# Optimization experiments

Hardware: AMD Instinct MI355X
Metric: run time of the kernel (lower is better)

The kernel has to match this reference:

```python
import jax, jax.numpy as jnp
import numpy as np

L, N, D, B_, T = 4, 4, 2048, 2, 2048  # num_blocks, expansion_rate, dim, batch, seq


def setup_inputs() -> dict:
    key = jax.random.key(0)
    ks = jax.random.split(key, 12)
    f = lambda k, sh, s=0.02: s * jax.random.normal(k, sh, jnp.float32)
    x = jax.random.normal(ks[0], (B_, T, D), jnp.float32)
    # structural torch inits + small noise so grads/kernels are exercised
    eyecols = jnp.stack([jnp.eye(N, dtype=jnp.float32)[:, [i % N]] for i in range(L)])  # [L,N,1]
    A_m = eyecols + f(ks[1], (L, N, 1), 0.05)
    A_r = jnp.broadcast_to(jnp.eye(N, dtype=jnp.float32), (L, N, N)) + f(ks[2], (L, N, N), 0.05)
    Bp = jnp.ones((L, 1, N), jnp.float32) + f(ks[3], (L, 1, N), 0.05)
    W_m = f(ks[4], (L, D, 1))
    W_r = f(ks[5], (L, D, N))
    W_b = f(ks[6], (L, D, N))
    s_a = 0.01 * jnp.ones((L, 1, 1), jnp.float32)
    s_b = 0.01 * jnp.ones((L, 1, 1), jnp.float32)
    dyn_gamma = jnp.ones((L, D), jnp.float32) + f(ks[7], (L, D), 0.05)   # LayerNorm(bias=False)
    norm_gamma = jnp.ones((L, D), jnp.float32) + f(ks[8], (L, D), 0.05)  # per-block norm weight
    norm_beta = f(ks[9], (L, D))                                          # per-block norm bias
    Wblk = f(ks[10], (L, D, D), 1.0) / np.sqrt(D)                         # block = Linear(D, D)
    bblk = f(ks[11], (L, D))
    return dict(x=x, A_m=A_m, A_r=A_r, Bp=Bp, W_m=W_m, W_r=W_r, W_b=W_b,
                s_a=s_a, s_b=s_b, dyn_gamma=dyn_gamma, norm_gamma=norm_gamma,
                norm_beta=norm_beta, Wblk=Wblk, bblk=bblk)


def _ln(x, gamma, beta=None, eps=1e-5):
    mu = jnp.mean(x, axis=-1, keepdims=True)
    var = jnp.mean(jnp.square(x - mu), axis=-1, keepdims=True)
    y = (x - mu) * jax.lax.rsqrt(var + eps) * gamma
    return y if beta is None else y + beta


def reference(x, A_m, A_r, Bp, W_m, W_r, W_b, s_a, s_b,
              dyn_gamma, norm_gamma, norm_beta, Wblk, bblk):
    # hyper branch (n > 0), dynamic=True, pre_norm=True
    H = jnp.repeat(x[:, :, None, :], N, axis=2)  # [B,T,N,D]
    for i in range(L):
        # ---- width connections ----
        Hn = _ln(H, dyn_gamma[i])                                              # dynamic LN, no bias
        Am = A_m[i] + s_a[i] * jnp.tanh(jnp.einsum('btnd,do->btno', Hn, W_m[i]))  # [B,T,N,1]
        Ar = A_r[i] + s_a[i] * jnp.tanh(jnp.einsum('btnd,dm->btnm', Hn, W_r[i]))  # [B,T,N,N]
        WC = jnp.concatenate([Am, Ar], axis=-1)                                # [B,T,N,1+N]
        Ht = jnp.einsum('btnd,btnm->btdm', H, WC)                              # H^T @ WC
        h = Ht[..., 0]                                                         # [B,T,D]
        H = jnp.swapaxes(Ht[..., 1:], -2, -1)                                  # [B,T,N,D]
        # ---- pre-norm + block ----
        h = _ln(h, norm_gamma[i], norm_beta[i])
        h = jnp.einsum('btd,de->bte', h, Wblk[i]) + bblk[i]
        # ---- depth connections ----
        hn = _ln(h, dyn_gamma[i])
        Bv = Bp[i][0] + s_b[i] * jnp.tanh(jnp.einsum('btd,dn->btn', hn, W_b[i]))  # [B,T,N]
        H = H + h[:, :, None, :] * Bv[..., None]
    return H.sum(axis=2)  # [B,T,D]
```

## Files before the change

kernel.cpp:

```cpp
#include <hip/hip_runtime.h>
#include <hip/hip_bf16.h>


#define DD 2048
#define NN 4
#define LL 4
#define NTOK 4096
#define EPSF 1e-5f
#define STS 80

typedef __attribute__((ext_vector_type(8))) short bf16x8;
typedef __attribute__((ext_vector_type(4))) float f32x4;
typedef __attribute__((ext_vector_type(2))) float f32x2;

__device__ __forceinline__ float bf2f(short u) {
  union { unsigned int i; float f; } v;
  v.i = ((unsigned int)(unsigned short)u) << 16;
  return v.f;
}
__device__ __forceinline__ short f2bf(float f) {
  __hip_bfloat16 h = __float2bfloat16(f);
  short s;
  __builtin_memcpy(&s, &h, 2);
  return s;
}
__device__ __forceinline__ float wred(float v) {
#pragma unroll
  for (int off = 32; off > 0; off >>= 1) v += __shfl_xor(v, off, 64);
  return v;
}
__device__ __forceinline__ void ld16(const void* g, void* l) {
  __builtin_amdgcn_global_load_lds(
      (const __attribute__((address_space(1))) void*)g,
      (__attribute__((address_space(3))) void*)l, 16, 0, 0);
}
__host__ __device__ constexpr int pofs(int k, int l) {
  return k == 0 ? 20 + l * 5
       : k == 1 ? 40 + (l - 1) * 5
       : k == 2 ? 55 + (l - 2) * 5
                : 65;
}

__global__ __launch_bounds__(256) void prep_pack(
    const float* __restrict__ W_m, const float* __restrict__ W_r,
    const float* __restrict__ W_b, const float* __restrict__ dyn_gamma,
    const float* __restrict__ norm_gamma, const float* __restrict__ norm_beta,
    short* __restrict__ gwm, short* __restrict__ gwr, short* __restrict__ gwb,
    float* __restrict__ rb) {
  const int i = blockIdx.x * 256 + threadIdx.x;
  const float g = dyn_gamma[i];
  gwm[i] = f2bf(g * W_m[i]);
  f32x4 r = *(const f32x4*)(W_r + (size_t)i * 4);
  f32x4 b = *(const f32x4*)(W_b + (size_t)i * 4);
  short ro[4], bo[4];
#pragma unroll
  for (int k = 0; k < 4; k++) { ro[k] = f2bf(g * r[k]); bo[k] = f2bf(g * b[k]); }
  *(unsigned long long*)(gwr + (size_t)i * 4) = *(unsigned long long*)ro;
  *(unsigned long long*)(gwb + (size_t)i * 4) = *(unsigned long long*)bo;
  rb[i] = norm_beta[i] / norm_gamma[i];
}

__global__ __launch_bounds__(64) void prep_sums(
    const float* __restrict__ W_m, const float* __restrict__ W_r,
    const float* __restrict__ W_b, const float* __restrict__ dyn_gamma,
    float* __restrict__ S0w, float* __restrict__ T0d) {
  const int l = blockIdx.x;
  const int lane = threadIdx.x;
  float s[5] = {0, 0, 0, 0, 0}, t[4] = {0, 0, 0, 0};
  for (int d = lane; d < DD; d += 64) {
    const float g = dyn_gamma[l * DD + d];
    s[0] += g * W_m[l * DD + d];
    f32x4 r = *(const f32x4*)(W_r + ((size_t)l * DD + d) * 4);
    f32x4 b = *(const f32x4*)(W_b + ((size_t)l * DD + d) * 4);
#pragma unroll
    for (int m = 0; m < 4; m++) { s[1 + m] += g * r[m]; t[m] += g * b[m]; }
  }
#pragma unroll
  for (int m = 0; m < 5; m++) s[m] = wred(s[m]);
#pragma unroll
  for (int n = 0; n < 4; n++) t[n] = wred(t[n]);
  if (lane == 0) {
#pragma unroll
    for (int m = 0; m < 5; m++) S0w[l * 5 + m] = s[m];
#pragma unroll
    for (int n = 0; n < 4; n++) T0d[l * 4 + n] = t[n];
  }
}

__global__ __launch_bounds__(256) void transpose_wblk(
    const float* __restrict__ W, const float* __restrict__ norm_gamma,
    short* __restrict__ Wt) {
  __shared__ float tile[64][65];
  const int blk = blockIdx.z;
  const int c0 = blockIdx.x * 64;
  const int r0 = blockIdx.y * 64;
  const float* Ws = W + (size_t)blk * DD * DD;
  short* Wd = Wt + (size_t)blk * DD * DD;
  const int tx = threadIdx.x & 63, ty = threadIdx.x >> 6;
#pragma unroll
  for (int r = 0; r < 16; r++) {
    const int row = ty + r * 4;
    tile[row][tx] = Ws[(size_t)(r0 + row) * DD + c0 + tx];
  }
  const float gsc = norm_gamma[blk * DD + r0 + tx];
  __syncthreads();
#pragma unroll
  for (int r = 0; r < 16; r++) {
    const int row = ty + r * 4;
    Wd[(size_t)(c0 + row) * DD + r0 + tx] = f2bf(tile[tx][row] * gsc);
  }
}

__global__ __launch_bounds__(256) void row_sums(
    const short* __restrict__ Wt, const float* __restrict__ rb,
    const float* __restrict__ bblk, float* __restrict__ E0,
    float* __restrict__ E1) {
  const int l = blockIdx.y;
  const int e = blockIdx.x * 4 + (threadIdx.x >> 6);
  const int lane = threadIdx.x & 63;
  const short* row = Wt + ((size_t)l * DD + e) * DD;
  const float* rbl = rb + l * DD;
  float s1 = 0.f, s0 = 0.f;
#pragma unroll
  for (int it = 0; it < 4; it++) {
    const int d0 = lane * 8 + it * 512;
    bf16x8 w = *(const bf16x8*)(row + d0);
    f32x4 r0 = *(const f32x4*)(rbl + d0), r1 = *(const f32x4*)(rbl + d0 + 4);
#pragma unroll
    for (int q = 0; q < 8; q++) {
      const float wq = bf2f(w[q]);
      s1 += wq;
      s0 += wq * ((q < 4) ? r0[q] : r1[q - 4]);
    }
  }
  s1 = wred(s1); s0 = wred(s0);
  if (lane == 0) {
    E1[l * DD + e] = s1;
    E0[l * DD + e] = s0 + bblk[l * DD + e];
  }
}

__global__ __launch_bounds__(256) void width0_kernel(
    const float* __restrict__ x, short* __restrict__ b0,
    short* __restrict__ hout, f32x2* __restrict__ tst, float* __restrict__ Cc,
    float* __restrict__ ST, const float* __restrict__ A_m,
    const float* __restrict__ A_r, const short* __restrict__ gwm,
    const short* __restrict__ gwr, const float* __restrict__ s_a,
    const float* __restrict__ S0w) {
  const int wave = threadIdx.x >> 6;
  const int lane = threadIdx.x & 63;
  const int tok = blockIdx.x * 4 + wave;
  const float* xr = x + (size_t)tok * DD;
  short* b0t = b0 + (size_t)tok * DD;

  bf16x8 xb[4];
#pragma unroll
  for (int j = 0; j < 4; j++) {
    const int d0 = lane * 8 + j * 512;
    f32x4 a = *(const f32x4*)(xr + d0);
    f32x4 b = *(const f32x4*)(xr + d0 + 4);
    bf16x8 p;
#pragma unroll
    for (int q = 0; q < 4; q++) { p[q] = f2bf(a[q]); p[4 + q] = f2bf(b[q]); }
    xb[j] = p;
    *(bf16x8*)(b0t + d0) = p;
  }

  float o = 0.f, qq = 0.f, P0[4][5];
#pragma unroll
  for (int l = 0; l < 4; l++)
#pragma unroll
    for (int m = 0; m < 5; m++) P0[l][m] = 0.f;

#pragma unroll
  for (int j = 0; j < 4; j++) {
    const int d0 = lane * 8 + j * 512;
    bf16x8 wmv[4], wrv[4][4];
#pragma unroll
    for (int l = 0; l < 4; l++) {
      wmv[l] = *(const bf16x8*)(gwm + l * DD + d0);
#pragma unroll
      for (int p = 0; p < 4; p++)
        wrv[l][p] = *(const bf16x8*)(gwr + ((size_t)l * DD + d0 + 2 * p) * 4);
    }
#pragma unroll
    for (int q = 0; q < 8; q++) {
      const float hv = bf2f(xb[j][q]);
      o += hv; qq += hv * hv;
#pragma unroll
      for (int l = 0; l < 4; l++) {
        P0[l][0] += hv * bf2f(wmv[l][q]);
#pragma unroll
        for (int m = 0; m < 4; m++)
          P0[l][1 + m] += hv * bf2f(wrv[l][q >> 1][(q & 1) * 4 + m]);
      }
    }
  }
  o = wred(o); qq = wred(qq);
#pragma unroll
  for (int l = 0; l < 4; l++)
#pragma unroll
    for (int m = 0; m < 5; m++) P0[l][m] = wred(P0[l][m]);

  const float sa = s_a[0];
  const float mu = o * (1.f / DD);
  const float inv = rsqrtf(qq * (1.f / DD) - mu * mu + EPSF);
  const float t0 = tanhf(inv * (P0[0][0] - mu * S0w[0]));
  float tm[4];
#pragma unroll
  for (int m = 0; m < 4; m++)
    tm[m] = tanhf(inv * (P0[0][1 + m] - mu * S0w[1 + m]));
  float amSum = 0.f, arCol[4] = {0, 0, 0, 0};
#pragma unroll
  for (int n = 0; n < 4; n++) {
    amSum += A_m[n] + sa * t0;
#pragma unroll
    for (int m = 0; m < 4; m++) arCol[m] += A_r[n * 4 + m] + sa * tm[m];
  }

  if (lane == 0) {
    const float sh = amSum * o;
    const float sh2 = amSum * amSum * qq;
    const float mu2 = sh * (1.f / DD);
    const float inv2 = rsqrtf(sh2 * (1.f / DD) - mu2 * mu2 + EPSF);
    f32x2 t; t[0] = inv2; t[1] = mu2 * inv2;
    tst[tok] = t;
    float* STt = ST + (size_t)tok * STS;
    STt[0] = o;
    STt[4] = qq;
#pragma unroll
    for (int l = 0; l < 4; l++)
#pragma unroll
      for (int m = 0; m < 5; m++) STt[pofs(0, l) + m] = P0[l][m];
    float* Ct = Cc + (size_t)tok * 16;
#pragma unroll
    for (int n = 0; n < 4; n++) Ct[n * 4] = arCol[n];
  }

  short* hw = hout + (size_t)tok * DD;
#pragma unroll
  for (int j = 0; j < 4; j++) {
    const int d0 = lane * 8 + j * 512;
    bf16x8 ho;
#pragma unroll
    for (int q = 0; q < 8; q++) ho[q] = f2bf(amSum * bf2f(xb[j][q]));
    *(bf16x8*)(hw + d0) = ho;
  }
}

__global__ __launch_bounds__(512) void gemm_kernel(
    const short* __restrict__ A, const short* __restrict__ Bt,
    const f32x2* __restrict__ tst, const float* __restrict__ E0,
    const float* __restrict__ E1, short* __restrict__ C) {
  __shared__ short lA[2][128 * 64];
  __shared__ short lB[2][128 * 64];
  const int tid = threadIdx.x;
  const int lane = tid & 63;
  const int wave = tid >> 6;
  const int bid = blockIdx.x;
  const int wg = (bid & 7) * 64 + (bid >> 3);
  const int m0 = (wg & 31) * 128, n0 = (wg >> 5) * 128;
  const int wm = wave >> 2;
  const int wn = wave & 3;

  f32x4 acc[4][2] = {};

#define STAGE(buf, kt)                                                        \
  {                                                                           \
    const int k0 = (kt) * 64;                                                 \
    _Pragma("unroll") for (int c = 0; c < 2; c++) {                           \
      const int idx = c * 512 + tid;                                          \
      const int row = idx >> 3;                                               \
      const int colsw = (((idx & 7) ^ (row & 7)) * 8);                        \
      ld16(A + (size_t)(m0 + row) * DD + k0 + colsw,                          \
           (char*)&lA[buf][0] + idx * 16);                                    \
      ld16(Bt + (size_t)(n0 + row) * DD + k0 + colsw,                         \
           (char*)&lB[buf][0] + idx * 16);                                    \
    }                                                                         \
  }

#define COMPUTE(cur)                                                          \
  {                                                                           \
    const char* bufA = (const char*)&lA[cur][0];                              \
    const char* bufB = (const char*)&lB[cur][0];                              \
    _Pragma("unroll") for (int kk = 0; kk < 2; ++kk) {                        \
      const int gsw = (kk * 64 + (lane >> 4) * 16) ^ ((lane & 7) << 4);       \
      bf16x8 af[4], bfr[2];                                                   \
      _Pragma("unroll") for (int m = 0; m < 4; m++) {                         \
        const int r = wm * 64 + m * 16 + (lane & 15);                         \
        af[m] = *(const bf16x8*)(bufA + r * 128 + gsw);                       \
      }                                                                       \
      _Pragma("unroll") for (int n = 0; n < 2; n++) {                         \
        const int r = wn * 32 + n * 16 + (lane & 15);                         \
        bfr[n] = *(const bf16x8*)(bufB + r * 128 + gsw);                      \
      }                                                                       \
      __builtin_amdgcn_s_setprio(1);                                          \
      _Pragma("unroll") for (int m = 0; m < 4; m++)                           \
        _Pragma("unroll") for (int n = 0; n < 2; n++)                         \
          acc[m][n] = __builtin_amdgcn_mfma_f32_16x16x32_bf16(                \
              af[m], bfr[n], acc[m][n], 0, 0, 0);                             \
      __builtin_amdgcn_s_setprio(0);                                          \
    }                                                                         \
  }

  STAGE(0, 0);
  for (int kt = 0; kt < 31; ++kt) {
    const int cur = kt & 1;
    STAGE(cur ^ 1, kt + 1);
    asm volatile("s_waitcnt vmcnt(4)" ::: "memory");
    asm volatile("s_barrier" ::: "memory");
    COMPUTE(cur);
    asm volatile("s_barrier" ::: "memory");
  }
  asm volatile("s_waitcnt vmcnt(0)" ::: "memory");
  asm volatile("s_barrier" ::: "memory");
  COMPUTE(1);
#undef STAGE
#undef COMPUTE

  float e0c[2], e1c[2];
  int cols[2];
#pragma unroll
  for (int n = 0; n < 2; n++) {
    cols[n] = n0 + wn * 32 + n * 16 + (lane & 15);
    e0c[n] = E0[cols[n]];
    e1c[n] = E1[cols[n]];
  }
#pragma unroll
  for (int m = 0; m < 4; m++) {
    const int rbase = m0 + wm * 64 + m * 16 + ((lane >> 4) << 2);
#pragma unroll
    for (int j = 0; j < 4; j++) {
      const int row = rbase + j;
      const f32x2 iv = tst[row];
#pragma unroll
      for (int n = 0; n < 2; n++)
        C[(size_t)row * DD + cols[n]] =
            f2bf(iv[0] * acc[m][n][j] - iv[1] * e1c[n] + e0c[n]);
    }
  }
}

template <int I>
__global__ __launch_bounds__(256) void fused_dw(
    const short* __restrict__ h2s, const short* __restrict__ b0,
    short* __restrict__ hout, f32x2* __restrict__ tst, float* __restrict__ Cc,
    float* __restrict__ ST, const float* __restrict__ Bp,
    const float* __restrict__ s_b, const float* __restrict__ A_m,
    const float* __restrict__ A_r, const float* __restrict__ s_a,
    const float* __restrict__ S0w, const float* __restrict__ T0d,
    const short* __restrict__ gwm, const short* __restrict__ gwr,
    const short* __restrict__ gwb) {
  constexpr int NB = I + 1;
  constexpr int NP = 3 - I;
  const int wave = threadIdx.x >> 6;
  const int lane = threadIdx.x & 63;
  const int tok = blockIdx.x * 4 + wave;

  const short* vt = h2s + ((size_t)I * NTOK + tok) * DD;
  const short* bases[I + 1];
  bases[0] = b0 + (size_t)tok * DD;
#pragma unroll
  for (int k = 1; k <= I; k++)
    bases[k] = h2s + ((size_t)(k - 1) * NTOK + tok) * DD;

  bf16x8 h2r[4];
#pragma unroll
  for (int j = 0; j < 4; j++)
    h2r[j] = *(const bf16x8*)(vt + lane * 8 + j * 512);

  float o = 0.f;
  float Gr[I + 2] = {};
  float Tb[4] = {0, 0, 0, 0};
  float Pn[NP][5];
#pragma unroll
  for (int li = 0; li < NP; li++)
#pragma unroll
    for (int m = 0; m < 5; m++) Pn[li][m] = 0.f;

#pragma unroll
  for (int j = 0; j < 4; j++) {
    const int d0 = lane * 8 + j * 512;
    bf16x8 bsv[I + 1];
#pragma unroll
    for (int k = 0; k <= I; k++) bsv[k] = *(const bf16x8*)(bases[k] + d0);
    bf16x8 wbv[4];
#pragma unroll
    for (int p = 0; p < 4; p++)
      wbv[p] = *(const bf16x8*)(gwb + ((size_t)I * DD + d0 + 2 * p) * 4);
    bf16x8 wmv[NP], wrv[NP][4];
#pragma unroll
    for (int li = 0; li < NP; li++) {
      const int l = NB + li;
      wmv[li] = *(const bf16x8*)(gwm + l * DD + d0);
#pragma unroll
      for (int p = 0; p < 4; p++)
        wrv[li][p] = *(const bf16x8*)(gwr + ((size_t)l * DD + d0 + 2 * p) * 4);
    }
#pragma unroll
    for (int q = 0; q < 8; q++) {
      const float hv = bf2f(h2r[j][q]);
      o += hv;
      Gr[I + 1] += hv * hv;
#pragma unroll
      for (int k = 0; k <= I; k++) Gr[k] += hv * bf2f(bsv[k][q]);
#pragma unroll
      for (int n = 0; n < 4; n++)
        Tb[n] += hv * bf2f(wbv[q >> 1][(q & 1) * 4 + n]);
#pragma unroll
      for (int li = 0; li < NP; li++) {
        Pn[li][0] += hv * bf2f(wmv[li][q]);
#pragma unroll
        for (int m = 0; m < 4; m++)
          Pn[li][1 + m] += hv * bf2f(wrv[li][q >> 1][(q & 1) * 4 + m]);
      }
    }
  }
  o = wred(o);
#pragma unroll
  for (int k = 0; k <= I + 1; k++) Gr[k] = wred(Gr[k]);
#pragma unroll
  for (int n = 0; n < 4; n++) Tb[n] = wred(Tb[n]);
#pragma unroll
  for (int li = 0; li < NP; li++)
#pragma unroll
    for (int m = 0; m < 5; m++) Pn[li][m] = wred(Pn[li][m]);

  float* STt = ST + (size_t)tok * STS;
  float* Ct = Cc + (size_t)tok * 16;
  float ofull[I + 2], Gf[I + 2][I + 2], Pf[I + 2][5], Cp[4][I + 2];
#pragma unroll
  for (int k = 0; k <= I; k++) ofull[k] = STt[k];
  ofull[I + 1] = o;
#pragma unroll
  for (int k = 0; k <= I; k++)
#pragma unroll
    for (int j2 = 0; j2 <= I; j2++) Gf[k][j2] = STt[4 + k * 4 + j2];
#pragma unroll
  for (int k = 0; k <= I; k++) { Gf[k][I + 1] = Gr[k]; Gf[I + 1][k] = Gr[k]; }
  Gf[I + 1][I + 1] = Gr[I + 1];
#pragma unroll
  for (int k = 0; k <= I; k++)
#pragma unroll
    for (int m = 0; m < 5; m++) Pf[k][m] = STt[pofs(k, NB) + m];
#pragma unroll
  for (int m = 0; m < 5; m++) Pf[I + 1][m] = Pn[0][m];
#pragma unroll
  for (int n = 0; n < 4; n++)
#pragma unroll
    for (int k = 0; k <= I; k++) Cp[n][k] = Ct[n * 4 + k];

  {
    const float mu2 = o * (1.f / DD);
    const float inv2 = rsqrtf(Gr[I + 1] * (1.f / DD) - mu2 * mu2 + EPSF);
    const float sb = s_b[I];
#pragma unroll
    for (int n = 0; n < 4; n++)
      Cp[n][I + 1] = Bp[I * 4 + n] +
                     sb * tanhf(inv2 * (Tb[n] - mu2 * T0d[I * 4 + n]));
  }

  const float sa = s_a[NB];
  float Am[4], Ar[4][4];
#pragma unroll
  for (int n = 0; n < 4; n++) {
    float sH = 0.f, sH2 = 0.f;
#pragma unroll
    for (int k = 0; k <= I + 1; k++) {
      sH += Cp[n][k] * ofull[k];
#pragma unroll
      for (int j2 = 0; j2 <= I + 1; j2++)
        sH2 += Cp[n][k] * Cp[n][j2] * Gf[k][j2];
    }
    const float mu = sH * (1.f / DD);
    const float inv = rsqrtf(sH2 * (1.f / DD) - mu * mu + EPSF);
    float S1[5];
#pragma unroll
    for (int m = 0; m < 5; m++) {
      S1[m] = 0.f;
#pragma unroll
      for (int k = 0; k <= I + 1; k++) S1[m] += Cp[n][k] * Pf[k][m];
    }
    Am[n] = A_m[NB * 4 + n] +
            sa * tanhf(inv * (S1[0] - mu * S0w[NB * 5 + 0]));
#pragma unroll
    for (int m = 0; m < 4; m++)
      Ar[n][m] = A_r[NB * 16 + n * 4 + m] +
                 sa * tanhf(inv * (S1[1 + m] - mu * S0w[NB * 5 + 1 + m]));
  }

  float Cn[4][I + 2], hc[I + 2];
#pragma unroll
  for (int k = 0; k <= I + 1; k++) {
    hc[k] = 0.f;
#pragma unroll
    for (int n = 0; n < 4; n++) hc[k] += Am[n] * Cp[n][k];
  }
#pragma unroll
  for (int mr = 0; mr < 4; mr++)
#pragma unroll
    for (int k = 0; k <= I + 1; k++) {
      float acc = 0.f;
#pragma unroll
      for (int n = 0; n < 4; n++) acc += Ar[n][mr] * Cp[n][k];
      Cn[mr][k] = acc;
    }

  if (lane == 0) {
    float sh = 0.f, sh2 = 0.f;
#pragma unroll
    for (int k = 0; k <= I + 1; k++) {
      sh += hc[k] * ofull[k];
#pragma unroll
      for (int j2 = 0; j2 <= I + 1; j2++) sh2 += hc[k] * hc[j2] * Gf[k][j2];
    }
    const float mu = sh * (1.f / DD);
    const float inv = rsqrtf(sh2 * (1.f / DD) - mu * mu + EPSF);
    f32x2 t; t[0] = inv; t[1] = mu * inv;
    tst[tok] = t;
    STt[I + 1] = o;
#pragma unroll
    for (int k = 0; k <= I + 1; k++) {
      STt[4 + (I + 1) * 4 + k] = Gf[I + 1][k];
      STt[4 + k * 4 + (I + 1)] = Gf[k][I + 1];
    }
#pragma unroll
    for (int li = 1; li < NP; li++)
#pragma unroll
      for (int m = 0; m < 5; m++) STt[pofs(I + 1, NB + li) + m] = Pn[li][m];
#pragma unroll
    for (int n = 0; n < 4; n++)
#pragma unroll
      for (int k = 0; k <= I + 1; k++) Ct[n * 4 + k] = Cn[n][k];
  }

  short* hw = hout + (size_t)tok * DD;
#pragma unroll
  for (int j = 0; j < 4; j++) {
    const int d0 = lane * 8 + j * 512;
    bf16x8 bsv[I + 1];
#pragma unroll
    for (int k = 0; k <= I; k++) bsv[k] = *(const bf16x8*)(bases[k] + d0);
    bf16x8 ho;
#pragma unroll
    for (int q = 0; q < 8; q++) {
      float a = hc[I + 1] * bf2f(h2r[j][q]);
#pragma unroll
      for (int k = 0; k <= I; k++) a += hc[k] * bf2f(bsv[k][q]);
      ho[q] = f2bf(a);
    }
    *(bf16x8*)(hw + d0) = ho;
  }
}

__global__ __launch_bounds__(256) void depth_last(
    const short* __restrict__ h2s, const short* __restrict__ b0,
    float* __restrict__ out, const float* __restrict__ Cc,
    const float* __restrict__ Bp, const float* __restrict__ s_b,
    const float* __restrict__ T0d, const short* __restrict__ gwb) {
  const int wave = threadIdx.x >> 6;
  const int lane = threadIdx.x & 63;
  const int tok = blockIdx.x * 4 + wave;
  const short* vt = h2s + ((size_t)3 * NTOK + tok) * DD;

  bf16x8 h2r[4];
  float s1 = 0.f, s2 = 0.f, Tb[4] = {0, 0, 0, 0};
#pragma unroll
  for (int j = 0; j < 4; j++) {
    const int d0 = lane * 8 + j * 512;
    h2r[j] = *(const bf16x8*)(vt + d0);
    bf16x8 wbv[4];
#pragma unroll
    for (int p = 0; p < 4; p++)
      wbv[p] = *(const bf16x8*)(gwb + ((size_t)3 * DD + d0 + 2 * p) * 4);
#pragma unroll
    for (int q = 0; q < 8; q++) {
      const float hv = bf2f(h2r[j][q]);
      s1 += hv; s2 += hv * hv;
#pragma unroll
      for (int n = 0; n < 4; n++)
        Tb[n] += hv * bf2f(wbv[q >> 1][(q & 1) * 4 + n]);
    }
  }
  s1 = wred(s1); s2 = wred(s2);
#pragma unroll
  for (int n = 0; n < 4; n++) Tb[n] = wred(Tb[n]);

  const float mu = s1 * (1.f / DD);
  const float inv = rsqrtf(s2 * (1.f / DD) - mu * mu + EPSF);
  const float sb = s_b[3];
  float bsum = 0.f;
#pragma unroll
  for (int n = 0; n < 4; n++)
    bsum += Bp[12 + n] + sb * tanhf(inv * (Tb[n] - mu * T0d[12 + n]));

  const float* Ct = Cc + (size_t)tok * 16;
  float e[4];
#pragma unroll
  for (int k = 0; k < 4; k++) {
    e[k] = 0.f;
#pragma unroll
    for (int n = 0; n < 4; n++) e[k] += Ct[n * 4 + k];
  }

  const short* bases[4];
  bases[0] = b0 + (size_t)tok * DD;
#pragma unroll
  for (int k = 1; k < 4; k++)
    bases[k] = h2s + ((size_t)(k - 1) * NTOK + tok) * DD;

  float* orow = out + (size_t)tok * DD;
#pragma unroll
  for (int j = 0; j < 4; j++) {
    const int d0 = lane * 8 + j * 512;
    bf16x8 bsv[4];
#pragma unroll
    for (int k = 0; k < 4; k++) bsv[k] = *(const bf16x8*)(bases[k] + d0);
    f32x4 o0, o1;
#pragma unroll
    for (int q = 0; q < 8; q++) {
      float s = bsum * bf2f(h2r[j][q]);
#pragma unroll
      for (int k = 0; k < 4; k++) s += e[k] * bf2f(bsv[k][q]);
      if (q < 4) o0[q] = s; else o1[q - 4] = s;
    }
    *(f32x4*)(orow + d0) = o0;
    *(f32x4*)(orow + d0 + 4) = o1;
  }
}

extern "C" void kernel_launch(void* const* d_in, const int* in_sizes, int n_in,
                              void* d_out, int out_size, void* d_ws,
                              size_t ws_size, hipStream_t stream) {
  const float* x = (const float*)d_in[0];
  const float* A_m = (const float*)d_in[1];
  const float* A_r = (const float*)d_in[2];
  const float* Bp = (const float*)d_in[3];
  const float* W_m = (const float*)d_in[4];
  const float* W_r = (const float*)d_in[5];
  const float* W_b = (const float*)d_in[6];
  const float* s_a = (const float*)d_in[7];
  const float* s_b = (const float*)d_in[8];
  const float* dyn_gamma = (const float*)d_in[9];
  const float* norm_gamma = (const float*)d_in[10];
  const float* norm_beta = (const float*)d_in[11];
  const float* Wblk = (const float*)d_in[12];
  const float* bblk = (const float*)d_in[13];
  float* out = (float*)d_out;

  char* ws = (char*)d_ws;
  short* b0 = (short*)(ws);
  short* h2s = (short*)(ws + 16777216);
  short* hnorm = (short*)(ws + 83886080);
  char* aux = ws + 100663296;
  short* gwm = (short*)(aux);
  short* gwr = (short*)(aux + 16384);
  short* gwb = (short*)(aux + 81920);
  float* rb = (float*)(aux + 147456);
  float* S0w = (float*)(aux + 180224);
  float* T0d = (float*)(aux + 181248);
  f32x2* tst = (f32x2*)(aux + 182272);
  float* E0 = (float*)(aux + 215040);
  float* E1 = (float*)(aux + 247808);
  float* Cc = (float*)(aux + 280576);
  float* ST = (float*)(aux + 542720);
  short* Wt = (short*)d_out;

  dim3 tb(256);
  prep_pack<<<32, tb, 0, stream>>>(W_m, W_r, W_b, dyn_gamma, norm_gamma,
                                   norm_beta, gwm, gwr, gwb, rb);
  prep_sums<<<4, dim3(64), 0, stream>>>(W_m, W_r, W_b, dyn_gamma, S0w, T0d);
  transpose_wblk<<<dim3(32, 32, 4), tb, 0, stream>>>(Wblk, norm_gamma, Wt);
  row_sums<<<dim3(512, 4), tb, 0, stream>>>(Wt, rb, bblk, E0, E1);
  width0_kernel<<<1024, tb, 0, stream>>>(x, b0, hnorm, tst, Cc, ST, A_m, A_r,
                                         gwm, gwr, s_a, S0w);
  for (int i = 0; i < LL; i++) {
    gemm_kernel<<<512, dim3(512), 0, stream>>>(
        hnorm, Wt + (size_t)i * DD * DD, tst, E0 + i * DD, E1 + i * DD,
        h2s + (size_t)i * NTOK * DD);
    if (i == 0)
      fused_dw<0><<<1024, tb, 0, stream>>>(h2s, b0, hnorm, tst, Cc, ST, Bp,
                                           s_b, A_m, A_r, s_a, S0w, T0d, gwm,
                                           gwr, gwb);
    else if (i == 1)
      fused_dw<1><<<1024, tb, 0, stream>>>(h2s, b0, hnorm, tst, Cc, ST, Bp,
                                           s_b, A_m, A_r, s_a, S0w, T0d, gwm,
                                           gwr, gwb);
    else if (i == 2)
      fused_dw<2><<<1024, tb, 0, stream>>>(h2s, b0, hnorm, tst, Cc, ST, Bp,
                                           s_b, A_m, A_r, s_a, S0w, T0d, gwm,
                                           gwr, gwb);
    else
      depth_last<<<1024, tb, 0, stream>>>(h2s, b0, out, Cc, Bp, s_b, T0d, gwb);
  }
}
```

Measured before the change: 326.6 us.

## Split each token across two waves in fused_dw and restructure GEMM K-loop sync

fused_dw now assigns two waves per token, each covering half of the 2048-wide row, and combines their partial reductions through shared memory with a block barrier. The grid doubles to 2048 blocks to give more parallelism and shorter per-wave serial work. The GEMM main loop also changes: it issues the next stage's loads, computes on the current buffer, then waits for all loads with vmcnt(0) and a single barrier, instead of a partial wait plus two barriers. This drops a barrier per iteration but makes each iteration wait for the prefetch to land, which may expose load latency.

```diff
diff --git a/kernel.cpp b/kernel.cpp
--- a/kernel.cpp
+++ b/kernel.cpp
@@ -304,17 +304,15 @@
   }
 
   STAGE(0, 0);
-  for (int kt = 0; kt < 31; ++kt) {
-    const int cur = kt & 1;
-    STAGE(cur ^ 1, kt + 1);
-    asm volatile("s_waitcnt vmcnt(4)" ::: "memory");
-    asm volatile("s_barrier" ::: "memory");
-    COMPUTE(cur);
-    asm volatile("s_barrier" ::: "memory");
-  }
   asm volatile("s_waitcnt vmcnt(0)" ::: "memory");
   asm volatile("s_barrier" ::: "memory");
-  COMPUTE(1);
+  for (int kt = 0; kt < 32; ++kt) {
+    const int cur = kt & 1;
+    if (kt < 31) STAGE(cur ^ 1, kt + 1);
+    COMPUTE(cur);
+    asm volatile("s_waitcnt vmcnt(0)" ::: "memory");
+    asm volatile("s_barrier" ::: "memory");
+  }
 #undef STAGE
 #undef COMPUTE
 
@@ -353,9 +351,16 @@
     const short* __restrict__ gwb) {
   constexpr int NB = I + 1;
   constexpr int NP = 3 - I;
+  constexpr int GO = 1;
+  constexpr int TO = I + 3;
+  constexpr int PO = I + 7;
+  __shared__ float red[2][2][24];
   const int wave = threadIdx.x >> 6;
   const int lane = threadIdx.x & 63;
-  const int tok = blockIdx.x * 4 + wave;
+  const int ti = wave >> 1;
+  const int wh = wave & 1;
+  const int tok = blockIdx.x * 2 + ti;
+  const int dbase = wh * 1024 + lane * 8;
 
   const short* vt = h2s + ((size_t)I * NTOK + tok) * DD;
   const short* bases[I + 1];
@@ -364,10 +369,10 @@
   for (int k = 1; k <= I; k++)
     bases[k] = h2s + ((size_t)(k - 1) * NTOK + tok) * DD;
 
-  bf16x8 h2r[4];
-#pragma unroll
-  for (int j = 0; j < 4; j++)
-    h2r[j] = *(const bf16x8*)(vt + lane * 8 + j * 512);
+  bf16x8 h2r[2];
+#pragma unroll
+  for (int j = 0; j < 2; j++)
+    h2r[j] = *(const bf16x8*)(vt + dbase + j * 512);
 
   float o = 0.f;
   float Gr[I + 2] = {};
@@ -379,8 +384,8 @@
     for (int m = 0; m < 5; m++) Pn[li][m] = 0.f;
 
 #pragma unroll
-  for (int j = 0; j < 4; j++) {
-    const int d0 = lane * 8 + j * 512;
+  for (int j = 0; j < 2; j++) {
+    const int d0 = dbase + j * 512;
     bf16x8 bsv[I + 1];
 #pragma unroll
     for (int k = 0; k <= I; k++) bsv[k] = *(const bf16x8*)(bases[k] + d0);
@@ -426,6 +431,34 @@
 #pragma unroll
     for (int m = 0; m < 5; m++) Pn[li][m] = wred(Pn[li][m]);
 
+  if (lane == 0) {
+    float* p = &red[ti][wh][0];
+    p[0] = o;
+#pragma unroll
+    for (int k = 0; k <= I + 1; k++) p[GO + k] = Gr[k];
+#pragma unroll
+    for (int n = 0; n < 4; n++) p[TO + n] = Tb[n];
+#pragma unroll
+    for (int li = 0; li < NP; li++)
+#pragma unroll
+      for (int m = 0; m < 5; m++) p[PO + li * 5 + m] = Pn[li][m];
+  }
+  __syncthreads();
+  {
+    const float* p0 = &red[ti][0][0];
+    const float* p1 = &red[ti][1][0];
+    o = p0[0] + p1[0];
+#pragma unroll
+    for (int k = 0; k <= I + 1; k++) Gr[k] = p0[GO + k] + p1[GO + k];
+#pragma unroll
+    for (int n = 0; n < 4; n++) Tb[n] = p0[TO + n] + p1[TO + n];
+#pragma unroll
+    for (int li = 0; li < NP; li++)
+#pragma unroll
+      for (int m = 0; m < 5; m++)
+        Pn[li][m] = p0[PO + li * 5 + m] + p1[PO + li * 5 + m];
+  }
+
   float* STt = ST + (size_t)tok * STS;
   float* Ct = Cc + (size_t)tok * 16;
   float ofull[I + 2], Gf[I + 2][I + 2], Pf[I + 2][5], Cp[4][I + 2];
@@ -506,7 +539,7 @@
       Cn[mr][k] = acc;
     }
 
-  if (lane == 0) {
+  if (wh == 0 && lane == 0) {
     float sh = 0.f, sh2 = 0.f;
 #pragma unroll
     for (int k = 0; k <= I + 1; k++) {
@@ -536,8 +569,8 @@
 
   short* hw = hout + (size_t)tok * DD;
 #pragma unroll
-  for (int j = 0; j < 4; j++) {
-    const int d0 = lane * 8 + j * 512;
+  for (int j = 0; j < 2; j++) {
+    const int d0 = dbase + j * 512;
     bf16x8 bsv[I + 1];
 #pragma unroll
     for (int k = 0; k <= I; k++) bsv[k] = *(const bf16x8*)(bases[k] + d0);
@@ -679,15 +712,15 @@
         hnorm, Wt + (size_t)i * DD * DD, tst, E0 + i * DD, E1 + i * DD,
         h2s + (size_t)i * NTOK * DD);
     if (i == 0)
-      fused_dw<0><<<1024, tb, 0, stream>>>(h2s, b0, hnorm, tst, Cc, ST, Bp,
+      fused_dw<0><<<2048, tb, 0, stream>>>(h2s, b0, hnorm, tst, Cc, ST, Bp,
                                            s_b, A_m, A_r, s_a, S0w, T0d, gwm,
                                            gwr, gwb);
     else if (i == 1)
-      fused_dw<1><<<1024, tb, 0, stream>>>(h2s, b0, hnorm, tst, Cc, ST, Bp,
+      fused_dw<1><<<2048, tb, 0, stream>>>(h2s, b0, hnorm, tst, Cc, ST, Bp,
                                            s_b, A_m, A_r, s_a, S0w, T0d, gwm,
                                            gwr, gwb);
     else if (i == 2)
-      fused_dw<2><<<1024, tb, 0, stream>>>(h2s, b0, hnorm, tst, Cc, ST, Bp,
+      fused_dw<2><<<2048, tb, 0, stream>>>(h2s, b0, hnorm, tst, Cc, ST, Bp,
                                            s_b, A_m, A_r, s_a, S0w, T0d, gwm,
                                            gwr, gwb);
     else
```

After: 338.7 us. 3.7% more time.

## Compute per-token weight projections with an MFMA table GEMM instead of scalar dots

Applied to the files above, without the earlier changes.

Packs all projection vectors (ones, gamma-scaled W_m, W_r, W_b for every layer) into a 48-column bf16 matrix in MFMA fragment order. A new table_dots kernel multiplies each layer's block output by this matrix with MFMA to get the row sums and all later-layer projections. fused_dw now reads those precomputed dots instead of doing scalar FMA loops over the weight vectors and writing partial products to ST. The cost is an extra kernel launch per layer and an extra TD buffer round trip through memory.

```diff
diff --git a/kernel.cpp b/kernel.cpp
--- a/kernel.cpp
+++ b/kernel.cpp
@@ -58,6 +58,64 @@
   *(unsigned long long*)(gwr + (size_t)i * 4) = *(unsigned long long*)ro;
   *(unsigned long long*)(gwb + (size_t)i * 4) = *(unsigned long long*)bo;
   rb[i] = norm_beta[i] / norm_gamma[i];
+}
+
+__global__ __launch_bounds__(256) void prep_tmf(
+    const short* __restrict__ gwm, const short* __restrict__ gwr,
+    const short* __restrict__ gwb, short* __restrict__ TMf) {
+  const int g = blockIdx.y;
+  const int kt = blockIdx.x * 4 + (threadIdx.x >> 6);
+  const int lane = threadIdx.x & 63;
+  const int col = g * 16 + (lane & 15);
+  const int k0 = kt * 32 + (lane >> 4) * 8;
+  short v[8];
+#pragma unroll
+  for (int j = 0; j < 8; j++) {
+    const int k = k0 + j;
+    short x = 0;
+    if (col == 0) x = (short)0x3F80;
+    else if (col <= 4) x = gwm[(col - 1) * DD + k];
+    else if (col <= 20) {
+      const int t = col - 5;
+      x = gwr[((size_t)(t >> 2) * DD + k) * 4 + (t & 3)];
+    } else if (col <= 36) {
+      const int t = col - 21;
+      x = gwb[((size_t)(t >> 2) * DD + k) * 4 + (t & 3)];
+    }
+    v[j] = x;
+  }
+  *(bf16x8*)(TMf + (size_t)((g * 64 + kt) * 64 + lane) * 8) = *(bf16x8*)v;
+}
+
+__global__ __launch_bounds__(64) void table_dots(
+    const short* __restrict__ v, const short* __restrict__ TMf,
+    float* __restrict__ TD) {
+  const int lane = threadIdx.x & 63;
+  const int tok0 = blockIdx.x * 16;
+  const char* ap = (const char*)(v + (size_t)(tok0 + (lane & 15)) * DD +
+                                 (lane >> 4) * 8);
+  f32x4 ac0 = {}, ac1 = {}, ac2 = {};
+#pragma unroll 4
+  for (int kt = 0; kt < 64; ++kt) {
+    bf16x8 a = *(const bf16x8*)(ap + kt * 64);
+    bf16x8 b0 = *(const bf16x8*)((const char*)TMf +
+                                 (size_t)((0 * 64 + kt) * 64 + lane) * 16);
+    bf16x8 b1 = *(const bf16x8*)((const char*)TMf +
+                                 (size_t)((1 * 64 + kt) * 64 + lane) * 16);
+    bf16x8 b2 = *(const bf16x8*)((const char*)TMf +
+                                 (size_t)((2 * 64 + kt) * 64 + lane) * 16);
+    ac0 = __builtin_amdgcn_mfma_f32_16x16x32_bf16(a, b0, ac0, 0, 0, 0);
+    ac1 = __builtin_amdgcn_mfma_f32_16x16x32_bf16(a, b1, ac1, 0, 0, 0);
+    ac2 = __builtin_amdgcn_mfma_f32_16x16x32_bf16(a, b2, ac2, 0, 0, 0);
+  }
+  const int trow = tok0 + ((lane >> 4) << 2);
+  const int c = lane & 15;
+#pragma unroll
+  for (int j = 0; j < 4; j++) {
+    TD[(size_t)(trow + j) * 48 + c] = ac0[j];
+    TD[(size_t)(trow + j) * 48 + 16 + c] = ac1[j];
+    TD[(size_t)(trow + j) * 48 + 32 + c] = ac2[j];
+  }
 }
 
 __global__ __launch_bounds__(64) void prep_sums(
@@ -345,14 +403,12 @@
 __global__ __launch_bounds__(256) void fused_dw(
     const short* __restrict__ h2s, const short* __restrict__ b0,
     short* __restrict__ hout, f32x2* __restrict__ tst, float* __restrict__ Cc,
-    float* __restrict__ ST, const float* __restrict__ Bp,
-    const float* __restrict__ s_b, const float* __restrict__ A_m,
-    const float* __restrict__ A_r, const float* __restrict__ s_a,
-    const float* __restrict__ S0w, const float* __restrict__ T0d,
-    const short* __restrict__ gwm, const short* __restrict__ gwr,
-    const short* __restrict__ gwb) {
+    float* __restrict__ ST, const float* __restrict__ TDs,
+    const float* __restrict__ Bp, const float* __restrict__ s_b,
+    const float* __restrict__ A_m, const float* __restrict__ A_r,
+    const float* __restrict__ s_a, const float* __restrict__ S0w,
+    const float* __restrict__ T0d) {
   constexpr int NB = I + 1;
-  constexpr int NP = 3 - I;
   const int wave = threadIdx.x >> 6;
   const int lane = threadIdx.x & 63;
   const int tok = blockIdx.x * 4 + wave;
@@ -369,69 +425,35 @@
   for (int j = 0; j < 4; j++)
     h2r[j] = *(const bf16x8*)(vt + lane * 8 + j * 512);
 
-  float o = 0.f;
   float Gr[I + 2] = {};
-  float Tb[4] = {0, 0, 0, 0};
-  float Pn[NP][5];
-#pragma unroll
-  for (int li = 0; li < NP; li++)
-#pragma unroll
-    for (int m = 0; m < 5; m++) Pn[li][m] = 0.f;
-
 #pragma unroll
   for (int j = 0; j < 4; j++) {
     const int d0 = lane * 8 + j * 512;
     bf16x8 bsv[I + 1];
 #pragma unroll
     for (int k = 0; k <= I; k++) bsv[k] = *(const bf16x8*)(bases[k] + d0);
-    bf16x8 wbv[4];
-#pragma unroll
-    for (int p = 0; p < 4; p++)
-      wbv[p] = *(const bf16x8*)(gwb + ((size_t)I * DD + d0 + 2 * p) * 4);
-    bf16x8 wmv[NP], wrv[NP][4];
-#pragma unroll
-    for (int li = 0; li < NP; li++) {
-      const int l = NB + li;
-      wmv[li] = *(const bf16x8*)(gwm + l * DD + d0);
-#pragma unroll
-      for (int p = 0; p < 4; p++)
-        wrv[li][p] = *(const bf16x8*)(gwr + ((size_t)l * DD + d0 + 2 * p) * 4);
-    }
 #pragma unroll
     for (int q = 0; q < 8; q++) {
       const float hv = bf2f(h2r[j][q]);
-      o += hv;
       Gr[I + 1] += hv * hv;
 #pragma unroll
       for (int k = 0; k <= I; k++) Gr[k] += hv * bf2f(bsv[k][q]);
-#pragma unroll
-      for (int n = 0; n < 4; n++)
-        Tb[n] += hv * bf2f(wbv[q >> 1][(q & 1) * 4 + n]);
-#pragma unroll
-      for (int li = 0; li < NP; li++) {
-        Pn[li][0] += hv * bf2f(wmv[li][q]);
-#pragma unroll
-        for (int m = 0; m < 4; m++)
-          Pn[li][1 + m] += hv * bf2f(wrv[li][q >> 1][(q & 1) * 4 + m]);
-      }
-    }
-  }
-  o = wred(o);
+    }
+  }
 #pragma unroll
   for (int k = 0; k <= I + 1; k++) Gr[k] = wred(Gr[k]);
-#pragma unroll
-  for (int n = 0; n < 4; n++) Tb[n] = wred(Tb[n]);
-#pragma unroll
-  for (int li = 0; li < NP; li++)
-#pragma unroll
-    for (int m = 0; m < 5; m++) Pn[li][m] = wred(Pn[li][m]);
 
   float* STt = ST + (size_t)tok * STS;
   float* Ct = Cc + (size_t)tok * 16;
+  const float* TDt[I + 1];
+#pragma unroll
+  for (int k = 0; k <= I; k++)
+    TDt[k] = TDs + ((size_t)k * NTOK + tok) * 48;
+
   float ofull[I + 2], Gf[I + 2][I + 2], Pf[I + 2][5], Cp[4][I + 2];
-#pragma unroll
-  for (int k = 0; k <= I; k++) ofull[k] = STt[k];
-  ofull[I + 1] = o;
+  ofull[0] = STt[0];
+#pragma unroll
+  for (int k = 1; k <= I + 1; k++) ofull[k] = TDt[k - 1][0];
 #pragma unroll
   for (int k = 0; k <= I; k++)
 #pragma unroll
@@ -440,18 +462,24 @@
   for (int k = 0; k <= I; k++) { Gf[k][I + 1] = Gr[k]; Gf[I + 1][k] = Gr[k]; }
   Gf[I + 1][I + 1] = Gr[I + 1];
 #pragma unroll
-  for (int k = 0; k <= I; k++)
-#pragma unroll
-    for (int m = 0; m < 5; m++) Pf[k][m] = STt[pofs(k, NB) + m];
-#pragma unroll
-  for (int m = 0; m < 5; m++) Pf[I + 1][m] = Pn[0][m];
+  for (int m = 0; m < 5; m++) Pf[0][m] = STt[pofs(0, NB) + m];
+#pragma unroll
+  for (int k = 1; k <= I + 1; k++) {
+    Pf[k][0] = TDt[k - 1][1 + NB];
+#pragma unroll
+    for (int m = 0; m < 4; m++) Pf[k][1 + m] = TDt[k - 1][5 + NB * 4 + m];
+  }
+  float Tb[4];
+#pragma unroll
+  for (int n = 0; n < 4; n++) Tb[n] = TDt[I][21 + I * 4 + n];
 #pragma unroll
   for (int n = 0; n < 4; n++)
 #pragma unroll
     for (int k = 0; k <= I; k++) Cp[n][k] = Ct[n * 4 + k];
 
   {
-    const float mu2 = o * (1.f / DD);
+    const float o_ = ofull[I + 1];
+    const float mu2 = o_ * (1.f / DD);
     const float inv2 = rsqrtf(Gr[I + 1] * (1.f / DD) - mu2 * mu2 + EPSF);
     const float sb = s_b[I];
 #pragma unroll
@@ -518,16 +546,11 @@
     const float inv = rsqrtf(sh2 * (1.f / DD) - mu * mu + EPSF);
     f32x2 t; t[0] = inv; t[1] = mu * inv;
     tst[tok] = t;
-    STt[I + 1] = o;
 #pragma unroll
     for (int k = 0; k <= I + 1; k++) {
       STt[4 + (I + 1) * 4 + k] = Gf[I + 1][k];
       STt[4 + k * 4 + (I + 1)] = Gf[k][I + 1];
     }
-#pragma unroll
-    for (int li = 1; li < NP; li++)
-#pragma unroll
-      for (int m = 0; m < 5; m++) STt[pofs(I + 1, NB + li) + m] = Pn[li][m];
 #pragma unroll
     for (int n = 0; n < 4; n++)
 #pragma unroll
@@ -664,11 +687,14 @@
   float* E1 = (float*)(aux + 247808);
   float* Cc = (float*)(aux + 280576);
   float* ST = (float*)(aux + 542720);
+  short* TMf = (short*)(aux + 2097152);
+  float* TDs = (float*)(aux + 2359296);
   short* Wt = (short*)d_out;
 
   dim3 tb(256);
   prep_pack<<<32, tb, 0, stream>>>(W_m, W_r, W_b, dyn_gamma, norm_gamma,
                                    norm_beta, gwm, gwr, gwb, rb);
+  prep_tmf<<<dim3(16, 3), tb, 0, stream>>>(gwm, gwr, gwb, TMf);
   prep_sums<<<4, dim3(64), 0, stream>>>(W_m, W_r, W_b, dyn_gamma, S0w, T0d);
   transpose_wblk<<<dim3(32, 32, 4), tb, 0, stream>>>(Wblk, norm_gamma, Wt);
   row_sums<<<dim3(512, 4), tb, 0, stream>>>(Wt, rb, bblk, E0, E1);
@@ -678,19 +704,20 @@
     gemm_kernel<<<512, dim3(512), 0, stream>>>(
         hnorm, Wt + (size_t)i * DD * DD, tst, E0 + i * DD, E1 + i * DD,
         h2s + (size_t)i * NTOK * DD);
-    if (i == 0)
-      fused_dw<0><<<1024, tb, 0, stream>>>(h2s, b0, hnorm, tst, Cc, ST, Bp,
-                                           s_b, A_m, A_r, s_a, S0w, T0d, gwm,
-                                           gwr, gwb);
-    else if (i == 1)
-      fused_dw<1><<<1024, tb, 0, stream>>>(h2s, b0, hnorm, tst, Cc, ST, Bp,
-                                           s_b, A_m, A_r, s_a, S0w, T0d, gwm,
-                                           gwr, gwb);
-    else if (i == 2)
-      fused_dw<2><<<1024, tb, 0, stream>>>(h2s, b0, hnorm, tst, Cc, ST, Bp,
-                                           s_b, A_m, A_r, s_a, S0w, T0d, gwm,
-                                           gwr, gwb);
-    else
+    if (i < LL - 1) {
+      table_dots<<<256, dim3(64), 0, stream>>>(
+          h2s + (size_t)i * NTOK * DD, TMf, TDs + (size_t)i * NTOK * 48);
+      if (i == 0)
+        fused_dw<0><<<1024, tb, 0, stream>>>(h2s, b0, hnorm, tst, Cc, ST, TDs,
+                                             Bp, s_b, A_m, A_r, s_a, S0w, T0d);
+      else if (i == 1)
+        fused_dw<1><<<1024, tb, 0, stream>>>(h2s, b0, hnorm, tst, Cc, ST, TDs,
+                                             Bp, s_b, A_m, A_r, s_a, S0w, T0d);
+      else
+        fused_dw<2><<<1024, tb, 0, stream>>>(h2s, b0, hnorm, tst, Cc, ST, TDs,
+                                             Bp, s_b, A_m, A_r, s_a, S0w, T0d);
+    } else {
       depth_last<<<1024, tb, 0, stream>>>(h2s, b0, out, Cc, Bp, s_b, T0d, gwb);
-  }
-}
+    }
+  }
+}
```

After: 357.7 us. 1.1x slower.
